# Optimization experiments

Measured on AMD Instinct MI355X. Metric: run time of the kernel, lower is better.

Reference implementation:

```python
import jax, jax.numpy as jnp
import numpy as np

SIM_K = 10.0
SIM_MID = 0.8
REF_SPECIES_INDEX = 0


def setup_inputs() -> dict:
    key = jax.random.key(0)
    k1, k2, k3, k4, k5 = jax.random.split(key, 5)
    B, L, M, A = 1, 256, 512, 21
    MSA = jax.random.uniform(k1, (B, L, M, A), dtype=jnp.float32)
    h = jax.random.normal(k2, (B, L, A), dtype=jnp.float32)
    J = jax.random.normal(k3, (B, L, L, A, A), dtype=jnp.float32)
    length_weight = jax.random.uniform(k4, (B, L, 1), dtype=jnp.float32)
    depth_weight = jax.random.uniform(k5, (B, M), dtype=jnp.float32)
    return {"MSA": MSA, "h": h, "J": J,
            "length_weight": length_weight, "depth_weight": depth_weight}


def reference(MSA, h, J, length_weight, depth_weight):
    # MSA: [B,L,M,A] -> [B,M,L,A]
    msa = jnp.einsum('blma->bmla', MSA)
    hb = h[:, None]  # [B,1,L,A]
    # Node energies
    H_node_wt = jnp.sum(msa * hb, axis=-1, keepdims=True)   # [B,M,L,1]
    H_node_diff = hb - H_node_wt                             # [B,M,L,A]
    # Edge energies: H_edge_mut[b,m,l,c] = sum_{p,a} MSA[b,m,p,a] * J[b,l,p,c,a]
    # (fuses the original ref-broadcast (M,l,L,A) tensor into a batched GEMM)
    H_edge_mut = jnp.einsum('bmpa,blpca->bmlc', msa, J)      # [B,M,L,A]
    H_edge_wt = jnp.sum(H_edge_mut * msa, axis=-1, keepdims=True)
    H_edge_diff = H_edge_mut - H_edge_wt
    H_diff = (H_node_diff + H_edge_diff)[..., :-1]           # drop gap state
    # Pseudo-likelihood per position
    logits = jax.nn.log_softmax(-H_diff, axis=-1)            # [B,M,L,A-1]
    logp_msa = jnp.sum(logits * msa[..., :-1], axis=-1)      # [B,M,L]
    # Sequence-similarity reweighting
    same_aa = jnp.einsum('bmla,bnla->bmnl', msa, msa)        # [B,M,M,L]
    same_aa = jnp.einsum('bmnl,bld->bmnd', same_aa, length_weight)
    sim = jnp.sum(same_aa, axis=-1) / jnp.sum(length_weight, axis=-2, keepdims=True)
    similarity_weight = 1.0 / jnp.sum(jax.nn.sigmoid(SIM_K * (sim - SIM_MID)), axis=-1)
    similarity_weight = similarity_weight * depth_weight     # [B,M]
    lp = jnp.einsum('bml,bld->bmd', logp_msa, length_weight)
    lp = jnp.sum(lp, axis=-1)                                # [B,M]
    logp = jnp.sum(similarity_weight * lp, axis=-1) / jnp.sum(similarity_weight, axis=-1)
    H_out = H_diff[:, REF_SPECIES_INDEX]                     # gather along M: [B,L,A-1]
    return (H_out, logp)
```

## Files before the change

kernel.cpp:

```cpp
#include <hip/hip_runtime.h>
#include <hip/hip_bf16.h>
#include <math.h>

#define LL_ 256
#define MM_ 512
#define AA_ 21
#define CC_ 20
#define KK_ (LL_*AA_)
#define SIM_K 10.0f
#define SIM_MID 0.8f

typedef __attribute__((ext_vector_type(8))) short bf16x8;
typedef __attribute__((ext_vector_type(4))) float f32x4;
#define MFMA16 __builtin_amdgcn_mfma_f32_16x16x32_bf16

static __device__ __forceinline__ unsigned short f2bf(float x) {
    union { float f; unsigned u; } v; v.f = x;
    unsigned r = v.u + 0x7fffu + ((v.u >> 16) & 1u);
    return (unsigned short)(r >> 16);
}
static __device__ __forceinline__ float bf2f(unsigned short h) {
    union { unsigned u; float f; } v; v.u = ((unsigned)h) << 16; return v.f;
}

#define B_JTHI  ((size_t)0)
#define B_JTLO  ((size_t)57802752)
#define B_AH    ((size_t)115605504)
#define B_AL    ((size_t)121110528)
#define B_HC    ((size_t)126615552)
#define B_MSAK  ((size_t)137625600)
#define B_LOGP  ((size_t)148635648)
#define B_S     ((size_t)149159936)
#define B_DENOM ((size_t)150208512)
#define B_LWSUM ((size_t)150210560)
#define WS_NEED ((size_t)150210564)

__global__ __launch_bounds__(256) void kT_jt(const float* __restrict__ J,
                                             unsigned short* __restrict__ Jt_hi,
                                             unsigned short* __restrict__ Jt_lo) {
    const int l = blockIdx.x;
    const int p0 = blockIdx.y * 32;
    const int tid = threadIdx.x;
    __shared__ float slab[32 * 441];
    const float* Jb = J + ((size_t)l * 256 + p0) * 441;
    for (int i = tid; i < 32 * 441; i += 256) slab[i] = Jb[i];
    __syncthreads();
    for (int s = tid; s < 21 * 84; s += 256) {
        const int c = s / 84;
        const int kk8 = s - c * 84;
        bf16x8 hv, lv;
#pragma unroll
        for (int j = 0; j < 8; ++j) {
            const int kseg = kk8 * 8 + j;
            const int pl = kseg / 21;
            const int a = kseg - pl * 21;
            const float x = slab[pl * 441 + c * 21 + a];
            const unsigned short h = f2bf(x);
            hv[j] = (short)h;
            lv[j] = (short)f2bf(x - bf2f(h));
        }
        const size_t row = (size_t)(l * 21 + c);
        const size_t off = row * KK_ + p0 * 21 + kk8 * 8;
        *(bf16x8*)(Jt_hi + off) = hv;
        *(bf16x8*)(Jt_lo + off) = lv;
    }
}

__global__ __launch_bounds__(512) void kA_msa(const float* __restrict__ MSA,
                                              unsigned short* __restrict__ Ah,
                                              unsigned short* __restrict__ Al) {
    const int p0 = blockIdx.x * 8;
    const int m0 = blockIdx.y * 64;
    const int tid = threadIdx.x;
    __shared__ float slab[8 * 64 * 21];
    for (int pl = 0; pl < 8; ++pl) {
        const float* src = MSA + ((size_t)(p0 + pl) * MM_ + m0) * AA_;
        for (int i = tid; i < 64 * 21; i += 512) slab[pl * 1344 + i] = src[i];
    }
    __syncthreads();
    const int ml = tid >> 3;
    const int pl = tid & 7;
    const size_t rowb = (size_t)(m0 + ml) * KK_ + (size_t)(p0 + pl) * 21;
#pragma unroll
    for (int a = 0; a < AA_; ++a) {
        const float x = slab[pl * 1344 + ml * 21 + a];
        const unsigned short h = f2bf(x);
        Ah[rowb + a] = h;
        Al[rowb + a] = f2bf(x - bf2f(h));
    }
}

#define K1M_AROW 136
__global__ __launch_bounds__(512, 2) __attribute__((amdgpu_waves_per_eu(2, 2)))
void k1_mfma(const unsigned short* __restrict__ Jt_hi,
             const unsigned short* __restrict__ Jt_lo,
             const unsigned short* __restrict__ Ah,
             const unsigned short* __restrict__ Al,
             float* __restrict__ Hc) {
    const int m0 = blockIdx.x * 128;
    const int lg = blockIdx.y;
    const int tid = threadIdx.x;
    const int lane = tid & 63;
    const int w = tid >> 6;
    const int wm = w >> 1;
    const int wn = w & 1;
    const int lr = lane & 15;
    const int lgk = lane >> 4;

    __shared__ unsigned short lds[(128 + 96) * K1M_AROW];
    const int BOFF = 128 * K1M_AROW;

    const int pl = (tid >> 3) & 1;
    const int gg = tid & 7;
    const int arow = tid >> 4;
    const unsigned short* Abase = pl ? Al : Ah;
    const unsigned short* Bbase = pl ? Jt_lo : Jt_hi;

    const unsigned short* sp0 = Abase + (size_t)(m0 + arow +  0) * KK_ + gg * 8;
    const unsigned short* sp1 = Abase + (size_t)(m0 + arow + 32) * KK_ + gg * 8;
    const unsigned short* sp2 = Abase + (size_t)(m0 + arow + 64) * KK_ + gg * 8;
    const unsigned short* sp3 = Abase + (size_t)(m0 + arow + 96) * KK_ + gg * 8;
    int br0 = lg * 84 + arow;       if (br0 > 5375) br0 = 5375;
    int br1 = lg * 84 + arow + 32;  if (br1 > 5375) br1 = 5375;
    int br2 = lg * 84 + arow + 64;  if (br2 > 5375) br2 = 5375;
    const unsigned short* sp4 = Bbase + (size_t)br0 * KK_ + gg * 8;
    const unsigned short* sp5 = Bbase + (size_t)br1 * KK_ + gg * 8;
    const unsigned short* sp6 = Bbase + (size_t)br2 * KK_ + gg * 8;

    const int dbase = arow * K1M_AROW + pl * 64 + gg * 8;
    const int dp0 = dbase;
    const int dp1 = dbase + 32 * K1M_AROW;
    const int dp2 = dbase + 64 * K1M_AROW;
    const int dp3 = dbase + 96 * K1M_AROW;
    const int dp4 = BOFF + dbase;
    const int dp5 = BOFF + dbase + 32 * K1M_AROW;
    const int dp6 = BOFF + dbase + 64 * K1M_AROW;

    f32x4 acc00 = (f32x4)(0.f), acc01 = (f32x4)(0.f), acc02 = (f32x4)(0.f);
    f32x4 acc10 = (f32x4)(0.f), acc11 = (f32x4)(0.f), acc12 = (f32x4)(0.f);

    int4 r0 = *(const int4*)sp0;
    int4 r1 = *(const int4*)sp1;
    int4 r2 = *(const int4*)sp2;
    int4 r3 = *(const int4*)sp3;
    int4 r4 = *(const int4*)sp4;
    int4 r5 = *(const int4*)sp5;
    int4 r6 = *(const int4*)sp6;

    for (int t = 0; t < 84; ++t) {
        *(int4*)&lds[dp0] = r0;
        *(int4*)&lds[dp1] = r1;
        *(int4*)&lds[dp2] = r2;
        *(int4*)&lds[dp3] = r3;
        *(int4*)&lds[dp4] = r4;
        *(int4*)&lds[dp5] = r5;
        *(int4*)&lds[dp6] = r6;
        __syncthreads();
        if (t < 83) {
            const size_t koff = (size_t)(t + 1) * 64;
            r0 = *(const int4*)(sp0 + koff);
            r1 = *(const int4*)(sp1 + koff);
            r2 = *(const int4*)(sp2 + koff);
            r3 = *(const int4*)(sp3 + koff);
            r4 = *(const int4*)(sp4 + koff);
            r5 = *(const int4*)(sp5 + koff);
            r6 = *(const int4*)(sp6 + koff);
        }
#pragma unroll
        for (int kc = 0; kc < 2; ++kc) {
            const int kb = kc * 32 + lgk * 8;
            const unsigned short* pa0 = &lds[(wm * 32 + lr) * K1M_AROW + kb];
            const unsigned short* pa1 = &lds[(wm * 32 + 16 + lr) * K1M_AROW + kb];
            const unsigned short* pb0 = &lds[BOFF + (wn * 48 + lr) * K1M_AROW + kb];
            const unsigned short* pb1 = &lds[BOFF + (wn * 48 + 16 + lr) * K1M_AROW + kb];
            const unsigned short* pb2 = &lds[BOFF + (wn * 48 + 32 + lr) * K1M_AROW + kb];
            const bf16x8 ah0 = *(const bf16x8*)pa0;
            const bf16x8 al0 = *(const bf16x8*)(pa0 + 64);
            const bf16x8 ah1 = *(const bf16x8*)pa1;
            const bf16x8 al1 = *(const bf16x8*)(pa1 + 64);
            const bf16x8 bh0 = *(const bf16x8*)pb0;
            const bf16x8 bl0 = *(const bf16x8*)(pb0 + 64);
            const bf16x8 bh1 = *(const bf16x8*)pb1;
            const bf16x8 bl1 = *(const bf16x8*)(pb1 + 64);
            const bf16x8 bh2 = *(const bf16x8*)pb2;
            const bf16x8 bl2 = *(const bf16x8*)(pb2 + 64);
            acc00 = MFMA16(ah0, bh0, acc00, 0, 0, 0);
            acc00 = MFMA16(ah0, bl0, acc00, 0, 0, 0);
            acc00 = MFMA16(al0, bh0, acc00, 0, 0, 0);
            acc01 = MFMA16(ah0, bh1, acc01, 0, 0, 0);
            acc01 = MFMA16(ah0, bl1, acc01, 0, 0, 0);
            acc01 = MFMA16(al0, bh1, acc01, 0, 0, 0);
            acc02 = MFMA16(ah0, bh2, acc02, 0, 0, 0);
            acc02 = MFMA16(ah0, bl2, acc02, 0, 0, 0);
            acc02 = MFMA16(al0, bh2, acc02, 0, 0, 0);
            acc10 = MFMA16(ah1, bh0, acc10, 0, 0, 0);
            acc10 = MFMA16(ah1, bl0, acc10, 0, 0, 0);
            acc10 = MFMA16(al1, bh0, acc10, 0, 0, 0);
            acc11 = MFMA16(ah1, bh1, acc11, 0, 0, 0);
            acc11 = MFMA16(ah1, bl1, acc11, 0, 0, 0);
            acc11 = MFMA16(al1, bh1, acc11, 0, 0, 0);
            acc12 = MFMA16(ah1, bh2, acc12, 0, 0, 0);
            acc12 = MFMA16(ah1, bl2, acc12, 0, 0, 0);
            acc12 = MFMA16(al1, bh2, acc12, 0, 0, 0);
        }
        __syncthreads();
    }
#define K1M_WRITE(ACC, MS, NS)                                                  \
    do {                                                                        \
        const int nloc = wn * 48 + (NS) * 16 + lr;                              \
        if (nloc < 84) {                                                        \
            const size_t ng = (size_t)lg * 84 + nloc;                           \
            const int mb = m0 + wm * 32 + (MS) * 16 + lgk * 4;                  \
            Hc[(size_t)(mb + 0) * KK_ + ng] = (ACC)[0];                         \
            Hc[(size_t)(mb + 1) * KK_ + ng] = (ACC)[1];                         \
            Hc[(size_t)(mb + 2) * KK_ + ng] = (ACC)[2];                         \
            Hc[(size_t)(mb + 3) * KK_ + ng] = (ACC)[3];                         \
        }                                                                       \
    } while (0)
    K1M_WRITE(acc00, 0, 0);
    K1M_WRITE(acc01, 0, 1);
    K1M_WRITE(acc02, 0, 2);
    K1M_WRITE(acc10, 1, 0);
    K1M_WRITE(acc11, 1, 1);
    K1M_WRITE(acc12, 1, 2);
#undef K1M_WRITE
}

#define OFF_MSAK   ((size_t)0)
#define OFF_HC     ((size_t)2752512)
#define OFF_LOGP   ((size_t)5505024)
#define OFF_S      ((size_t)5636096)
#define OFF_DENOM  ((size_t)5898240)
#define OFF_LWSUM  ((size_t)5898752)

__global__ __launch_bounds__(256) void k0_transpose(const float* __restrict__ MSA,
                                                    float* __restrict__ msa_k) {
    const int l = blockIdx.x;
    const int m = blockIdx.y * 256 + threadIdx.x;
    const float* src = MSA + ((size_t)l * MM_ + m) * AA_;
#pragma unroll
    for (int a = 0; a < AA_; ++a) msa_k[(size_t)(l * AA_ + a) * MM_ + m] = src[a];
}

__global__ __launch_bounds__(256) void k_lwsum(const float* __restrict__ lw,
                                               float* __restrict__ out) {
    const int t = threadIdx.x;
    float v = lw[t];
#pragma unroll
    for (int off = 32; off; off >>= 1) v += __shfl_down(v, off, 64);
    __shared__ float r[4];
    if ((t & 63) == 0) r[t >> 6] = v;
    __syncthreads();
    if (t == 0) out[0] = r[0] + r[1] + r[2] + r[3];
}

#define K1_BL 4
#define K1_BM 128
#define K1_PP 4
__global__ __launch_bounds__(512) void k1_edge(const float* __restrict__ Jg,
                                               const float* __restrict__ msa_k,
                                               float* __restrict__ Hc) {
    const int m0 = blockIdx.x * K1_BM;
    const int l0 = blockIdx.y * K1_BL;
    const int tid = threadIdx.x;
    const int mq = tid & 31;
    const int nq = tid >> 5;
    __shared__ float Jl[K1_PP][AA_][96];
    float acc[6][4];
#pragma unroll
    for (int j = 0; j < 6; ++j)
#pragma unroll
        for (int i = 0; i < 4; ++i) acc[j][i] = 0.f;
    const int nj = (nq < 4) ? 6 : 5;
    for (int p0 = 0; p0 < LL_; p0 += K1_PP) {
        __syncthreads();
        for (int idx = tid; idx < K1_BL * K1_PP * 441; idx += 512) {
            const int pair = idx / 441;
            const int f = idx - pair * 441;
            const int ll = pair >> 2;
            const int pp = pair & 3;
            const int c = f / 21;
            const int a = f - c * 21;
            Jl[pp][a][ll * 21 + c] =
                Jg[(size_t)(l0 + ll) * (LL_ * AA_ * AA_) + (size_t)(p0 + pp) * 441 + f];
        }
        __syncthreads();
#pragma unroll
        for (int pp = 0; pp < K1_PP; ++pp) {
#pragma unroll 7
            for (int a = 0; a < AA_; ++a) {
                const int k = (p0 + pp) * AA_ + a;
                const float4 av = *(const float4*)(msa_k + (size_t)k * MM_ + m0 + (mq << 2));
#pragma unroll
                for (int j = 0; j < 6; ++j) {
                    const float b = Jl[pp][a][nq + 16 * j];
                    acc[j][0] = fmaf(av.x, b, acc[j][0]);
                    acc[j][1] = fmaf(av.y, b, acc[j][1]);
                    acc[j][2] = fmaf(av.z, b, acc[j][2]);
                    acc[j][3] = fmaf(av.w, b, acc[j][3]);
                }
            }
        }
    }
    for (int j = 0; j < nj; ++j) {
        const int n = nq + 16 * j;
        const int ll = n / 21;
        const int c = n - ll * 21;
        const int l = l0 + ll;
#pragma unroll
        for (int i = 0; i < 4; ++i) {
            const int m = m0 + (mq << 2) + i;
            Hc[((size_t)m * LL_ + l) * AA_ + c] = acc[j][i];
        }
    }
}

__global__ __launch_bounds__(512) void k2_node(const float* __restrict__ MSA,
                                               const float* __restrict__ hvec,
                                               const float* __restrict__ Hc,
                                               float* __restrict__ logp,
                                               float* __restrict__ out) {
    const int l = blockIdx.x;
    const int m = threadIdx.x;
    __shared__ float hl[AA_];
    if (m < AA_) hl[m] = hvec[l * AA_ + m];
    __syncthreads();
    const float* msa = MSA + ((size_t)l * MM_ + m) * AA_;
    const float* hc = Hc + ((size_t)m * LL_ + l) * AA_;
    float msav[AA_], hcv[AA_];
#pragma unroll
    for (int a = 0; a < AA_; ++a) { msav[a] = msa[a]; hcv[a] = hc[a]; }
    float nodewt = 0.f, edgewt = 0.f;
#pragma unroll
    for (int a = 0; a < AA_; ++a) {
        nodewt = fmaf(msav[a], hl[a], nodewt);
        edgewt = fmaf(msav[a], hcv[a], edgewt);
    }
    float hd[CC_];
    float mx = -1e30f;
#pragma unroll
    for (int c = 0; c < CC_; ++c) {
        hd[c] = (hl[c] - nodewt) + (hcv[c] - edgewt);
        mx = fmaxf(mx, -hd[c]);
    }
    float s = 0.f;
#pragma unroll
    for (int c = 0; c < CC_; ++c) s += expf(-hd[c] - mx);
    const float lse = mx + logf(s);
    float lpsum = 0.f;
#pragma unroll
    for (int c = 0; c < CC_; ++c) lpsum = fmaf(-hd[c] - lse, msav[c], lpsum);
    logp[l * MM_ + m] = lpsum;
    if (m == 0) {
#pragma unroll
        for (int c = 0; c < CC_; ++c) out[l * CC_ + c] = hd[c];
    }
}

__global__ __launch_bounds__(256) void k3_sim(const float* __restrict__ msa_k,
                                              const float* __restrict__ lw,
                                              float* __restrict__ S) {
    const int m0 = blockIdx.x * 64;
    const int n0 = blockIdx.y * 64;
    const int l0 = blockIdx.z * 32;
    const int tid = threadIdx.x;
    const int tx = tid & 15;
    const int ty = tid >> 4;
    __shared__ __align__(16) float As[21][64];
    __shared__ __align__(16) float Bs[21][64];
    float acc[4][4];
#pragma unroll
    for (int i = 0; i < 4; ++i)
#pragma unroll
        for (int j = 0; j < 4; ++j) acc[i][j] = 0.f;
    for (int l = l0; l < l0 + 32; ++l) {
        __syncthreads();
        const float lwv = lw[l];
        for (int idx = tid; idx < 21 * 64; idx += 256) {
            const int kk = idx >> 6, mm = idx & 63;
            const size_t row = (size_t)(l * 21 + kk) * MM_;
            As[kk][mm] = msa_k[row + m0 + mm];
            Bs[kk][mm] = msa_k[row + n0 + mm] * lwv;
        }
        __syncthreads();
#pragma unroll 7
        for (int kk = 0; kk < 21; ++kk) {
            const float4 a4 = *(const float4*)&As[kk][tx * 4];
            const float4 b4 = *(const float4*)&Bs[kk][ty * 4];
            const float av[4] = {a4.x, a4.y, a4.z, a4.w};
            const float bv[4] = {b4.x, b4.y, b4.z, b4.w};
#pragma unroll
            for (int i = 0; i < 4; ++i)
#pragma unroll
                for (int j = 0; j < 4; ++j)
                    acc[i][j] = fmaf(av[i], bv[j], acc[i][j]);
        }
    }
#pragma unroll
    for (int i = 0; i < 4; ++i)
#pragma unroll
        for (int j = 0; j < 4; ++j)
            atomicAdd(&S[(size_t)(m0 + tx * 4 + i) * MM_ + n0 + ty * 4 + j], acc[i][j]);
}

__global__ __launch_bounds__(64) void k4_denom(const float* __restrict__ S,
                                               const float* __restrict__ lwsum_p,
                                               float* __restrict__ denom) {
    const int m = blockIdx.x * 64 + threadIdx.x;
    const float inv = 1.0f / lwsum_p[0];
    float s = 0.f;
    for (int n = 0; n < MM_; ++n) {
        const float sim = S[(size_t)n * MM_ + m] * inv;
        s += 1.0f / (1.0f + expf(-SIM_K * (sim - SIM_MID)));
    }
    denom[m] = s;
}

__global__ __launch_bounds__(512) void k5_final(const float* __restrict__ logp,
                                                const float* __restrict__ lw,
                                                const float* __restrict__ denom,
                                                const float* __restrict__ dw,
                                                float* __restrict__ out) {
    const int m = threadIdx.x;
    float lp = 0.f;
    for (int l = 0; l < LL_; ++l) lp = fmaf(logp[l * MM_ + m], lw[l], lp);
    const float sw = dw[m] / denom[m];
    float a = sw * lp, b = sw;
#pragma unroll
    for (int off = 32; off; off >>= 1) {
        a += __shfl_down(a, off, 64);
        b += __shfl_down(b, off, 64);
    }
    __shared__ float ra[8], rb[8];
    if ((m & 63) == 0) { ra[m >> 6] = a; rb[m >> 6] = b; }
    __syncthreads();
    if (m == 0) {
        float sa = 0.f, sb = 0.f;
#pragma unroll
        for (int w = 0; w < 8; ++w) { sa += ra[w]; sb += rb[w]; }
        out[5120] = sa / sb;
    }
}

extern "C" void kernel_launch(void* const* d_in, const int* in_sizes, int n_in,
                              void* d_out, int out_size, void* d_ws, size_t ws_size,
                              hipStream_t stream) {
    const float* MSA = (const float*)d_in[0];
    const float* h   = (const float*)d_in[1];
    const float* J   = (const float*)d_in[2];
    const float* lw  = (const float*)d_in[3];
    const float* dw  = (const float*)d_in[4];
    float* out = (float*)d_out;

    if (ws_size >= WS_NEED) {
        char* wsb = (char*)d_ws;
        unsigned short* Jt_hi = (unsigned short*)(wsb + B_JTHI);
        unsigned short* Jt_lo = (unsigned short*)(wsb + B_JTLO);
        unsigned short* Ah    = (unsigned short*)(wsb + B_AH);
        unsigned short* Al    = (unsigned short*)(wsb + B_AL);
        float* Hc    = (float*)(wsb + B_HC);
        float* msa_k = (float*)(wsb + B_MSAK);
        float* logp  = (float*)(wsb + B_LOGP);
        float* S     = (float*)(wsb + B_S);
        float* denom = (float*)(wsb + B_DENOM);
        float* lwsum = (float*)(wsb + B_LWSUM);

        kT_jt<<<dim3(LL_, 8), 256, 0, stream>>>(J, Jt_hi, Jt_lo);
        kA_msa<<<dim3(32, 8), 512, 0, stream>>>(MSA, Ah, Al);
        k0_transpose<<<dim3(LL_, MM_ / 256), 256, 0, stream>>>(MSA, msa_k);
        k_lwsum<<<1, 256, 0, stream>>>(lw, lwsum);
        hipMemsetAsync(S, 0, (size_t)MM_ * MM_ * sizeof(float), stream);
        k1_mfma<<<dim3(4, 64), 512, 0, stream>>>(Jt_hi, Jt_lo, Ah, Al, Hc);
        k3_sim<<<dim3(8, 8, 8), 256, 0, stream>>>(msa_k, lw, S);
        k2_node<<<dim3(LL_), 512, 0, stream>>>(MSA, h, Hc, logp, out);
        k4_denom<<<dim3(MM_ / 64), 64, 0, stream>>>(S, lwsum, denom);
        k5_final<<<1, 512, 0, stream>>>(logp, lw, denom, dw, out);
    } else {
        float* ws = (float*)d_ws;
        float* msa_k = ws + OFF_MSAK;
        float* Hc    = ws + OFF_HC;
        float* logp  = ws + OFF_LOGP;
        float* S     = ws + OFF_S;
        float* denom = ws + OFF_DENOM;
        float* lwsum = ws + OFF_LWSUM;
        k0_transpose<<<dim3(LL_, MM_ / 256), 256, 0, stream>>>(MSA, msa_k);
        k_lwsum<<<1, 256, 0, stream>>>(lw, lwsum);
        hipMemsetAsync(S, 0, (size_t)MM_ * MM_ * sizeof(float), stream);
        k1_edge<<<dim3(MM_ / K1_BM, LL_ / K1_BL), 512, 0, stream>>>(J, msa_k, Hc);
        k3_sim<<<dim3(8, 8, 8), 256, 0, stream>>>(msa_k, lw, S);
        k2_node<<<dim3(LL_), 512, 0, stream>>>(MSA, h, Hc, logp, out);
        k4_denom<<<dim3(MM_ / 64), 64, 0, stream>>>(S, lwsum, denom);
        k5_final<<<1, 512, 0, stream>>>(logp, lw, denom, dw, out);
    }
}
```

Before: 558.7 us.

## Split-K the MFMA edge GEMM across two blocks with atomic accumulation

```diff
diff --git a/kernel.cpp b/kernel.cpp
--- a/kernel.cpp
+++ b/kernel.cpp
@@ -42,8 +42,9 @@
     const int p0 = blockIdx.y * 32;
     const int tid = threadIdx.x;
     __shared__ float slab[32 * 441];
-    const float* Jb = J + ((size_t)l * 256 + p0) * 441;
-    for (int i = tid; i < 32 * 441; i += 256) slab[i] = Jb[i];
+    const float4* Jb4 = (const float4*)(J + ((size_t)l * 256 + p0) * 441);
+    float4* slab4 = (float4*)slab;
+    for (int i = tid; i < (32 * 441) / 4; i += 256) slab4[i] = Jb4[i];
     __syncthreads();
     for (int s = tid; s < 21 * 84; s += 256) {
         const int c = s / 84;
@@ -91,7 +92,7 @@
 }
 
 #define K1M_AROW 136
-__global__ __launch_bounds__(512, 2) __attribute__((amdgpu_waves_per_eu(2, 2)))
+__global__ __launch_bounds__(512, 4) __attribute__((amdgpu_waves_per_eu(4)))
 void k1_mfma(const unsigned short* __restrict__ Jt_hi,
              const unsigned short* __restrict__ Jt_lo,
              const unsigned short* __restrict__ Ah,
@@ -99,6 +100,7 @@
              float* __restrict__ Hc) {
     const int m0 = blockIdx.x * 128;
     const int lg = blockIdx.y;
+    const int ks = blockIdx.z;
     const int tid = threadIdx.x;
     const int lane = tid & 63;
     const int w = tid >> 6;
@@ -115,17 +117,18 @@
     const int arow = tid >> 4;
     const unsigned short* Abase = pl ? Al : Ah;
     const unsigned short* Bbase = pl ? Jt_lo : Jt_hi;
-
-    const unsigned short* sp0 = Abase + (size_t)(m0 + arow +  0) * KK_ + gg * 8;
-    const unsigned short* sp1 = Abase + (size_t)(m0 + arow + 32) * KK_ + gg * 8;
-    const unsigned short* sp2 = Abase + (size_t)(m0 + arow + 64) * KK_ + gg * 8;
-    const unsigned short* sp3 = Abase + (size_t)(m0 + arow + 96) * KK_ + gg * 8;
+    const size_t k0 = (size_t)ks * 42 * 64;
+
+    const unsigned short* sp0 = Abase + (size_t)(m0 + arow +  0) * KK_ + k0 + gg * 8;
+    const unsigned short* sp1 = Abase + (size_t)(m0 + arow + 32) * KK_ + k0 + gg * 8;
+    const unsigned short* sp2 = Abase + (size_t)(m0 + arow + 64) * KK_ + k0 + gg * 8;
+    const unsigned short* sp3 = Abase + (size_t)(m0 + arow + 96) * KK_ + k0 + gg * 8;
     int br0 = lg * 84 + arow;       if (br0 > 5375) br0 = 5375;
     int br1 = lg * 84 + arow + 32;  if (br1 > 5375) br1 = 5375;
     int br2 = lg * 84 + arow + 64;  if (br2 > 5375) br2 = 5375;
-    const unsigned short* sp4 = Bbase + (size_t)br0 * KK_ + gg * 8;
-    const unsigned short* sp5 = Bbase + (size_t)br1 * KK_ + gg * 8;
-    const unsigned short* sp6 = Bbase + (size_t)br2 * KK_ + gg * 8;
+    const unsigned short* sp4 = Bbase + (size_t)br0 * KK_ + k0 + gg * 8;
+    const unsigned short* sp5 = Bbase + (size_t)br1 * KK_ + k0 + gg * 8;
+    const unsigned short* sp6 = Bbase + (size_t)br2 * KK_ + k0 + gg * 8;
 
     const int dbase = arow * K1M_AROW + pl * 64 + gg * 8;
     const int dp0 = dbase;
@@ -147,7 +150,7 @@
     int4 r5 = *(const int4*)sp5;
     int4 r6 = *(const int4*)sp6;
 
-    for (int t = 0; t < 84; ++t) {
+    for (int t = 0; t < 42; ++t) {
         *(int4*)&lds[dp0] = r0;
         *(int4*)&lds[dp1] = r1;
         *(int4*)&lds[dp2] = r2;
@@ -156,7 +159,7 @@
         *(int4*)&lds[dp5] = r5;
         *(int4*)&lds[dp6] = r6;
         __syncthreads();
-        if (t < 83) {
+        if (t < 41) {
             const size_t koff = (size_t)(t + 1) * 64;
             r0 = *(const int4*)(sp0 + koff);
             r1 = *(const int4*)(sp1 + koff);
@@ -211,10 +214,10 @@
         if (nloc < 84) {                                                        \
             const size_t ng = (size_t)lg * 84 + nloc;                           \
             const int mb = m0 + wm * 32 + (MS) * 16 + lgk * 4;                  \
-            Hc[(size_t)(mb + 0) * KK_ + ng] = (ACC)[0];                         \
-            Hc[(size_t)(mb + 1) * KK_ + ng] = (ACC)[1];                         \
-            Hc[(size_t)(mb + 2) * KK_ + ng] = (ACC)[2];                         \
-            Hc[(size_t)(mb + 3) * KK_ + ng] = (ACC)[3];                         \
+            atomicAdd(&Hc[(size_t)(mb + 0) * KK_ + ng], (ACC)[0]);              \
+            atomicAdd(&Hc[(size_t)(mb + 1) * KK_ + ng], (ACC)[1]);              \
+            atomicAdd(&Hc[(size_t)(mb + 2) * KK_ + ng], (ACC)[2]);              \
+            atomicAdd(&Hc[(size_t)(mb + 3) * KK_ + ng], (ACC)[3]);              \
         }                                                                       \
     } while (0)
     K1M_WRITE(acc00, 0, 0);
@@ -470,7 +473,8 @@
         k0_transpose<<<dim3(LL_, MM_ / 256), 256, 0, stream>>>(MSA, msa_k);
         k_lwsum<<<1, 256, 0, stream>>>(lw, lwsum);
         hipMemsetAsync(S, 0, (size_t)MM_ * MM_ * sizeof(float), stream);
-        k1_mfma<<<dim3(4, 64), 512, 0, stream>>>(Jt_hi, Jt_lo, Ah, Al, Hc);
+        hipMemsetAsync(Hc, 0, (size_t)MM_ * KK_ * sizeof(float), stream);
+        k1_mfma<<<dim3(4, 64, 2), 512, 0, stream>>>(Jt_hi, Jt_lo, Ah, Al, Hc);
         k3_sim<<<dim3(8, 8, 8), 256, 0, stream>>>(msa_k, lw, S);
         k2_node<<<dim3(LL_), 512, 0, stream>>>(MSA, h, Hc, logp, out);
         k4_denom<<<dim3(MM_ / 64), 64, 0, stream>>>(S, lwsum, denom);
```

Result: faster. 547.2 us (-2.1%).
